# Kernel tuning notes

Measured on AMD Instinct MI355X. Metric: run time of the kernel, lower is better.

The kernel has to match this reference:

```python
import jax, jax.numpy as jnp
import numpy as np

N = 100000      # nodes
E = 1600000     # edges (avg degree 16)
F_IN = 128
H1, H2, C = 200, 50, 10


def _lin(key, fin, fout):
    # Glorot-uniform-ish init
    lim = (6.0 / (fin + fout)) ** 0.5
    return jax.random.uniform(key, (fin, fout), jnp.float32, -lim, lim)


def setup_inputs() -> dict:
    key = jax.random.key(0)
    ks = jax.random.split(key, 11)
    x = jax.random.normal(ks[0], (N, F_IN), jnp.float32)
    edge_index = jax.random.randint(ks[1], (2, E), 0, N, jnp.int32)
    return {
        "x": x,
        "edge_index": edge_index,
        "W_l1": _lin(ks[2], F_IN, H1), "b1": jnp.zeros((H1,), jnp.float32), "W_r1": _lin(ks[3], F_IN, H1),
        "W_l2": _lin(ks[4], H1, H2),   "b2": jnp.zeros((H2,), jnp.float32), "W_r2": _lin(ks[5], H1, H2),
        "W_l3": _lin(ks[6], H2, C),    "b3": jnp.zeros((C,), jnp.float32),  "W_r3": _lin(ks[7], H2, C),
    }


def _sage_conv_max(x, src, dst, W_l, b, W_r):
    # gather neighbor (source) features, scatter-max into destination nodes
    agg = jax.ops.segment_max(x[src], dst, num_segments=N)   # [N, F]
    agg = jnp.where(jnp.isfinite(agg), agg, 0.0)             # empty segments -> 0 (PyG behavior)
    return agg @ W_l + b + x @ W_r


def reference(x, edge_index, W_l1, b1, W_r1, W_l2, b2, W_r2, W_l3, b3, W_r3):
    src, dst = edge_index[0], edge_index[1]
    h = _sage_conv_max(x, src, dst, W_l1, b1, W_r1)   # [N, 200]
    h = _sage_conv_max(h, src, dst, W_l2, b2, W_r2)   # [N, 50]
    h = _sage_conv_max(h, src, dst, W_l3, b3, W_r3)   # [N, 10]
    return jax.nn.log_softmax(h, axis=1)
```

## Files before the change

### kernel.cpp

```cpp
#include <hip/hip_runtime.h>
#include <cstdint>
#include <cstddef>

#define N_NODES 100000
#define N_EDGES 1600000
#define F_IN    128
#define H1D     200
#define H2D     50
#define NCLS    10

#define P1 256
#define P2 416
#define P3 128
#define H2OFF 56

#define BSH 9
#define BMASK 511
#define NB 196
#define EPB 8192

typedef __attribute__((ext_vector_type(8))) short short8;
typedef __attribute__((ext_vector_type(4))) float f32x4;

__device__ __forceinline__ unsigned short f2b(float f) {
    union { float f; uint32_t u; } v; v.f = f;
    uint32_t u = v.u;
    return (unsigned short)((u + 0x7fffu + ((u >> 16) & 1u)) >> 16);
}
__device__ __forceinline__ float b2f(unsigned short b) {
    union { uint32_t u; float f; } v; v.u = ((uint32_t)b) << 16;
    return v.f;
}
__device__ __forceinline__ void upk(uint32_t p, float& a, float& b) {
    union { uint32_t u; float f; } lo, hi;
    lo.u = (p & 0xffffu) << 16;
    hi.u = p & 0xffff0000u;
    a = lo.f; b = hi.f;
}

__global__ void hist_kernel(const int* __restrict__ dst, int* __restrict__ deg, int E) {
    int e = blockIdx.x * blockDim.x + threadIdx.x;
    if (e < E) atomicAdd(&deg[dst[e]], 1);
}

__device__ __forceinline__ int block_excl_scan_256(int v, int* wsum) {
    const int tid = threadIdx.x;
    const int lane = tid & 63;
    const int wid = tid >> 6;
    int incl = v;
    #pragma unroll
    for (int off = 1; off < 64; off <<= 1) {
        int t = __shfl_up(incl, off, 64);
        if (lane >= off) incl += t;
    }
    if (lane == 63) wsum[wid] = incl;
    __syncthreads();
    if (tid == 0) {
        int s = 0;
        #pragma unroll
        for (int k = 0; k < 4; k++) { int t = wsum[k]; wsum[k] = s; s += t; }
    }
    __syncthreads();
    return wsum[wid] + incl - v;
}

__global__ __launch_bounds__(256) void scan_k1(const int* __restrict__ deg,
                                               int* __restrict__ row_ptr,
                                               int* __restrict__ bsum, int N) {
    __shared__ int wsum[4];
    const int tid = threadIdx.x;
    const int base = blockIdx.x * 1024 + tid * 4;
    int v[4];
    #pragma unroll
    for (int k = 0; k < 4; k++) v[k] = (base + k < N) ? deg[base + k] : 0;
    int t = v[0] + v[1] + v[2] + v[3];
    int texcl = block_excl_scan_256(t, wsum);
    int run = texcl;
    #pragma unroll
    for (int k = 0; k < 4; k++) {
        if (base + k < N) row_ptr[base + k] = run;
        run += v[k];
    }
    if (tid == 255) bsum[blockIdx.x] = texcl + t;
}

__global__ __launch_bounds__(256) void scan_k2(int* __restrict__ bsum, int NBLK) {
    __shared__ int wsum[4];
    const int tid = threadIdx.x;
    int v = (tid < NBLK) ? bsum[tid] : 0;
    int excl = block_excl_scan_256(v, wsum);
    if (tid < NBLK) bsum[tid] = excl;
}

__global__ __launch_bounds__(256) void scan_k3(int* __restrict__ row_ptr,
                                               const int* __restrict__ bsum, int N) {
    int add = bsum[blockIdx.x];
    int base = blockIdx.x * 1024 + threadIdx.x * 4;
    #pragma unroll
    for (int k = 0; k < 4; k++)
        if (base + k < N) row_ptr[base + k] += add;
}

__global__ void scan_k4(int* __restrict__ row_ptr, int* __restrict__ g_bcur, int N, int E) {
    int tid = threadIdx.x;
    if (tid == 0) row_ptr[N] = E;
    if (tid < NB) g_bcur[tid] = row_ptr[tid << BSH];
}

__global__ __launch_bounds__(256) void fill_pass1(const int* __restrict__ src,
                                                  const int* __restrict__ dst,
                                                  int* __restrict__ g_bcur,
                                                  uint32_t* __restrict__ staging, int E) {
    __shared__ int cnt[256];
    __shared__ int base_s[256];
    const int tid = threadIdx.x;
    const int base = blockIdx.x * EPB;
    cnt[tid] = 0;
    __syncthreads();
    #pragma unroll 4
    for (int i = 0; i < EPB / 256; i++) {
        int e = base + i * 256 + tid;
        if (e < E) atomicAdd(&cnt[dst[e] >> BSH], 1);
    }
    __syncthreads();
    int v = cnt[tid];
    if (v > 0) base_s[tid] = atomicAdd(&g_bcur[tid], v);
    cnt[tid] = 0;
    __syncthreads();
    #pragma unroll 4
    for (int i = 0; i < EPB / 256; i++) {
        int e = base + i * 256 + tid;
        if (e < E) {
            int d = dst[e], s = src[e];
            int b = d >> BSH;
            int r = atomicAdd(&cnt[b], 1);
            staging[base_s[b] + r] = ((uint32_t)s << BSH) | (uint32_t)(d & BMASK);
        }
    }
}

__global__ __launch_bounds__(256) void fill_pass2(const uint32_t* __restrict__ staging,
                                                  const int* __restrict__ row_ptr,
                                                  int* __restrict__ col_src, int N) {
    __shared__ int lcur[512];
    const int tid = threadIdx.x;
    const int nodeBase = blockIdx.x << BSH;
    for (int i = tid; i < 512; i += 256) {
        int node = nodeBase + i;
        lcur[i] = (node < N) ? row_ptr[node] : 0;
    }
    __syncthreads();
    const int lo = row_ptr[nodeBase];
    const int nodeEnd = min(nodeBase + 512, N);
    const int hi = row_ptr[nodeEnd];
    for (int j = lo + tid; j < hi; j += 256) {
        uint32_t rec = staging[j];
        int dl = rec & BMASK;
        int s  = (int)(rec >> BSH);
        int p = atomicAdd(&lcur[dl], 1);
        col_src[p] = s;
    }
}

__global__ void build_bt_kernel(const float* __restrict__ Wl, const float* __restrict__ Wr,
                                unsigned short* __restrict__ Bt,
                                int K1, int k2off, int K2, int M, int P) {
    int idx = blockIdx.x * blockDim.x + threadIdx.x;
    if (idx >= M * P) return;
    int m = idx / P, k = idx - m * P;
    float v = 0.0f;
    if (k < K1)                          v = Wl[(size_t)k * M + m];
    else if (k >= k2off && k < k2off+K2) v = Wr[(size_t)(k - k2off) * M + m];
    Bt[(size_t)m * P + k] = f2b(v);
}

__global__ void conv_x_kernel(const float* __restrict__ x, unsigned short* __restrict__ A1, int N) {
    int idx = blockIdx.x * blockDim.x + threadIdx.x;
    if (idx >= N * 32) return;
    int row = idx >> 5, c4 = (idx & 31) * 4;
    float4 v = *(const float4*)(x + (size_t)row * F_IN + c4);
    ushort4 o;
    o.x = f2b(v.x); o.y = f2b(v.y); o.z = f2b(v.z); o.w = f2b(v.w);
    *(ushort4*)(A1 + (size_t)row * P1 + F_IN + c4) = o;
}

__global__ void pad_zero_kernel(unsigned short* __restrict__ A, int pitch,
                                int begin, int width, int N) {
    int idx = blockIdx.x * blockDim.x + threadIdx.x;
    if (idx >= N * width) return;
    int r = idx / width, c = idx - r * width;
    A[(size_t)r * pitch + begin + c] = 0;
}

template <int F, int G>
__global__ __launch_bounds__(256) void agg_max_v2(
    const unsigned short* __restrict__ X, int xpitch,
    const int* __restrict__ row_ptr, const int* __restrict__ col_src,
    unsigned short* __restrict__ O, int opitch, int N) {
    static_assert(G == 8 || G == 16 || G == 32, "G must be 8/16/32");
    static_assert(G * 8 >= F, "group must cover F");
    const int wave = (blockIdx.x * blockDim.x + threadIdx.x) >> 6;
    const int lane = threadIdx.x & 63;
    if (wave >= N) return;
    const int beg = row_ptr[wave];
    const int end = row_ptr[wave + 1];
    constexpr int LOG2G = (G == 8) ? 3 : ((G == 16) ? 4 : 5);
    constexpr int EPW = 64 / G;
    const int l = lane & (G - 1);
    const int grp = lane >> LOG2G;
    const int f0 = l * 8;
    const bool act = (f0 < F);

    float m[8];
    #pragma unroll
    for (int i = 0; i < 8; i++) m[i] = -INFINITY;

    auto body = [&](int s) {
        if (act) {
            const uint4 v = *(const uint4*)(X + (size_t)s * xpitch + f0);
            float a, b;
            upk(v.x, a, b); m[0] = fmaxf(m[0], a); m[1] = fmaxf(m[1], b);
            upk(v.y, a, b); m[2] = fmaxf(m[2], a); m[3] = fmaxf(m[3], b);
            upk(v.z, a, b); m[4] = fmaxf(m[4], a); m[5] = fmaxf(m[5], b);
            upk(v.w, a, b); m[6] = fmaxf(m[6], a); m[7] = fmaxf(m[7], b);
        }
    };

    int j = beg + grp;
    for (; j + EPW < end; j += 2 * EPW) {
        int s0 = col_src[j];
        int s1 = col_src[j + EPW];
        body(s0);
        body(s1);
    }
    if (j < end) body(col_src[j]);

    #pragma unroll
    for (int off = G; off < 64; off <<= 1) {
        #pragma unroll
        for (int i = 0; i < 8; i++)
            m[i] = fmaxf(m[i], __shfl_xor(m[i], off, 64));
    }

    if (grp == 0 && act) {
        unsigned short* op = O + (size_t)wave * opitch;
        const bool empty = (beg == end);
        if (f0 + 8 <= F) {
            uint4 o = {0u, 0u, 0u, 0u};
            if (!empty) {
                o.x = (uint32_t)f2b(m[0]) | ((uint32_t)f2b(m[1]) << 16);
                o.y = (uint32_t)f2b(m[2]) | ((uint32_t)f2b(m[3]) << 16);
                o.z = (uint32_t)f2b(m[4]) | ((uint32_t)f2b(m[5]) << 16);
                o.w = (uint32_t)f2b(m[6]) | ((uint32_t)f2b(m[7]) << 16);
            }
            *(uint4*)(op + f0) = o;
        } else {
            for (int i = 0; f0 + i < F; i++)
                op[f0 + i] = empty ? (unsigned short)0 : f2b(m[i]);
        }
    }
}

__global__ __launch_bounds__(256) void gemm_mfma_kernel(
    const unsigned short* __restrict__ A, int P,
    const unsigned short* __restrict__ Bt,
    const float* __restrict__ bias,
    float* __restrict__ Cf,
    unsigned short* __restrict__ Cb, int cbPitch, int cbOff,
    int Nrows, int M) {
    __shared__ short As[64 * 40];
    __shared__ short Bs[64 * 40];
    const int tid = threadIdx.x;
    const int wv = tid >> 6;
    const int lane = tid & 63;
    const int q = lane >> 4;
    const int mi = lane & 15;
    const int rowBase = blockIdx.x * 64;
    const int colBase = blockIdx.y * 64;

    f32x4 acc[4];
    #pragma unroll
    for (int c = 0; c < 4; c++) acc[c] = (f32x4){0.f, 0.f, 0.f, 0.f};

    const int srow = tid >> 2;
    const int sseg = tid & 3;
    const int grow = rowBase + srow;
    const int gcol = colBase + srow;

    for (int kt = 0; kt < P; kt += 32) {
        uint4 va = {0u, 0u, 0u, 0u};
        uint4 vb = {0u, 0u, 0u, 0u};
        if (grow < Nrows) va = *(const uint4*)(A + (size_t)grow * P + kt + sseg * 8);
        if (gcol < M)     vb = *(const uint4*)(Bt + (size_t)gcol * P + kt + sseg * 8);
        *(uint4*)(&As[srow * 40 + sseg * 8]) = va;
        *(uint4*)(&Bs[srow * 40 + sseg * 8]) = vb;
        __syncthreads();
        short8 a = *(const short8*)(&As[(wv * 16 + mi) * 40 + q * 8]);
        #pragma unroll
        for (int c = 0; c < 4; c++) {
            short8 b = *(const short8*)(&Bs[(c * 16 + mi) * 40 + q * 8]);
            acc[c] = __builtin_amdgcn_mfma_f32_16x16x32_bf16(a, b, acc[c], 0, 0, 0);
        }
        __syncthreads();
    }

    #pragma unroll
    for (int c = 0; c < 4; c++) {
        int col = colBase + c * 16 + mi;
        if (col >= M) continue;
        float bv = bias[col];
        #pragma unroll
        for (int r = 0; r < 4; r++) {
            int row = rowBase + wv * 16 + q * 4 + r;
            if (row >= Nrows) continue;
            float v = acc[c][r] + bv;
            if (Cf) Cf[(size_t)row * M + col] = v;
            else    Cb[(size_t)row * cbPitch + cbOff + col] = f2b(v);
        }
    }
}

__global__ void logsoftmax_kernel(float* __restrict__ io, int N) {
    int n = blockIdx.x * blockDim.x + threadIdx.x;
    if (n >= N) return;
    float v[NCLS];
    float m = -INFINITY;
    #pragma unroll
    for (int i = 0; i < NCLS; i++) { v[i] = io[(size_t)n * NCLS + i]; m = fmaxf(m, v[i]); }
    float s = 0.0f;
    #pragma unroll
    for (int i = 0; i < NCLS; i++) s += expf(v[i] - m);
    float ls = logf(s);
    #pragma unroll
    for (int i = 0; i < NCLS; i++) io[(size_t)n * NCLS + i] = v[i] - m - ls;
}

extern "C" void kernel_launch(void* const* d_in, const int* in_sizes, int n_in,
                              void* d_out, int out_size, void* d_ws, size_t ws_size,
                              hipStream_t stream) {
    const float* x    = (const float*)d_in[0];
    const int*   eidx = (const int*)d_in[1];
    const float* Wl1  = (const float*)d_in[2];
    const float* b1   = (const float*)d_in[3];
    const float* Wr1  = (const float*)d_in[4];
    const float* Wl2  = (const float*)d_in[5];
    const float* b2   = (const float*)d_in[6];
    const float* Wr2  = (const float*)d_in[7];
    const float* Wl3  = (const float*)d_in[8];
    const float* b3   = (const float*)d_in[9];
    const float* Wr3  = (const float*)d_in[10];
    const int* srcp = eidx;
    const int* dstp = eidx + N_EDGES;
    float* out = (float*)d_out;
    (void)ws_size; (void)in_sizes; (void)n_in; (void)out_size;

    char* w = (char*)d_ws;
    size_t off = 0;
    auto alloc = [&](size_t bytes) -> char* {
        char* p = w + off;
        off += (bytes + 255) & ~(size_t)255;
        return p;
    };
    int* deg      = (int*)alloc(sizeof(int) * N_NODES);
    int* row_ptr  = (int*)alloc(sizeof(int) * (N_NODES + 1));
    int* col_src  = (int*)alloc(sizeof(int) * N_EDGES);
    uint32_t* staging = (uint32_t*)alloc(sizeof(uint32_t) * N_EDGES);
    int* bsum     = (int*)alloc(sizeof(int) * 128);
    int* g_bcur   = (int*)alloc(sizeof(int) * 256);
    unsigned short* A1  = (unsigned short*)alloc(sizeof(short) * (size_t)N_NODES * P1);
    unsigned short* A2  = (unsigned short*)alloc(sizeof(short) * (size_t)N_NODES * P2);
    unsigned short* A3  = (unsigned short*)alloc(sizeof(short) * (size_t)N_NODES * P3);
    unsigned short* Bt1 = (unsigned short*)alloc(sizeof(short) * H1D * P1);
    unsigned short* Bt2 = (unsigned short*)alloc(sizeof(short) * H2D * P2);
    unsigned short* Bt3 = (unsigned short*)alloc(sizeof(short) * NCLS * P3);

    const int SCAN_BLKS = (N_NODES + 1023) / 1024;
    hipMemsetAsync(deg, 0, sizeof(int) * N_NODES, stream);
    hist_kernel<<<(N_EDGES + 255) / 256, 256, 0, stream>>>(dstp, deg, N_EDGES);
    scan_k1<<<SCAN_BLKS, 256, 0, stream>>>(deg, row_ptr, bsum, N_NODES);
    scan_k2<<<1, 256, 0, stream>>>(bsum, SCAN_BLKS);
    scan_k3<<<SCAN_BLKS, 256, 0, stream>>>(row_ptr, bsum, N_NODES);
    scan_k4<<<1, 256, 0, stream>>>(row_ptr, g_bcur, N_NODES, N_EDGES);
    fill_pass1<<<(N_EDGES + EPB - 1) / EPB, 256, 0, stream>>>(srcp, dstp, g_bcur, staging, N_EDGES);
    fill_pass2<<<NB, 256, 0, stream>>>(staging, row_ptr, col_src, N_NODES);

    build_bt_kernel<<<(H1D * P1 + 255) / 256, 256, 0, stream>>>(Wl1, Wr1, Bt1, F_IN, F_IN, F_IN, H1D, P1);
    build_bt_kernel<<<(H2D * P2 + 255) / 256, 256, 0, stream>>>(Wl2, Wr2, Bt2, H1D, H1D, H1D, H2D, P2);
    build_bt_kernel<<<(NCLS * P3 + 255) / 256, 256, 0, stream>>>(Wl3, Wr3, Bt3, H2D, H2OFF, H2D, NCLS, P3);
    conv_x_kernel<<<(N_NODES * 32 + 255) / 256, 256, 0, stream>>>(x, A1, N_NODES);
    pad_zero_kernel<<<(N_NODES * 16 + 255) / 256, 256, 0, stream>>>(A2, P2, 2 * H1D, P2 - 2 * H1D, N_NODES);
    pad_zero_kernel<<<(N_NODES * 6 + 255) / 256, 256, 0, stream>>>(A3, P3, H2D, H2OFF - H2D, N_NODES);
    pad_zero_kernel<<<(N_NODES * 22 + 255) / 256, 256, 0, stream>>>(A3, P3, H2OFF + H2D, P3 - H2OFF - H2D, N_NODES);

    const int aggBlocks = (N_NODES + 3) / 4;
    const int rowTiles = (N_NODES + 63) / 64;

    agg_max_v2<F_IN, 16><<<aggBlocks, 256, 0, stream>>>(A1 + F_IN, P1, row_ptr, col_src, A1, P1, N_NODES);
    dim3 g1(rowTiles, (H1D + 63) / 64);
    gemm_mfma_kernel<<<g1, 256, 0, stream>>>(A1, P1, Bt1, b1, nullptr, A2, P2, H1D, N_NODES, H1D);

    agg_max_v2<H1D, 32><<<aggBlocks, 256, 0, stream>>>(A2 + H1D, P2, row_ptr, col_src, A2, P2, N_NODES);
    dim3 g2(rowTiles, 1);
    gemm_mfma_kernel<<<g2, 256, 0, stream>>>(A2, P2, Bt2, b2, nullptr, A3, P3, H2OFF, N_NODES, H2D);

    agg_max_v2<H2D, 8><<<aggBlocks, 256, 0, stream>>>(A3 + H2OFF, P3, row_ptr, col_src, A3, P3, N_NODES);
    dim3 g3(rowTiles, 1);
    gemm_mfma_kernel<<<g3, 256, 0, stream>>>(A3, P3, Bt3, b3, out, nullptr, 0, 0, N_NODES, NCLS);

    logsoftmax_kernel<<<(N_NODES + 255) / 256, 256, 0, stream>>>(out, N_NODES);
}
```

Baseline: 576.6 us.

## Restructure CSR build, unroll aggregation loads, widen GEMM tiles to full output

```diff
diff --git a/kernel.cpp b/kernel.cpp
--- a/kernel.cpp
+++ b/kernel.cpp
@@ -38,11 +38,6 @@
     a = lo.f; b = hi.f;
 }
 
-__global__ void hist_kernel(const int* __restrict__ dst, int* __restrict__ deg, int E) {
-    int e = blockIdx.x * blockDim.x + threadIdx.x;
-    if (e < E) atomicAdd(&deg[dst[e]], 1);
-}
-
 __device__ __forceinline__ int block_excl_scan_256(int v, int* wsum) {
     const int tid = threadIdx.x;
     const int lane = tid & 63;
@@ -64,53 +59,38 @@
     return wsum[wid] + incl - v;
 }
 
-__global__ __launch_bounds__(256) void scan_k1(const int* __restrict__ deg,
-                                               int* __restrict__ row_ptr,
-                                               int* __restrict__ bsum, int N) {
+__global__ __launch_bounds__(256) void csr_p0(const int* __restrict__ dst,
+                                              int* __restrict__ bcnt, int E) {
+    __shared__ int c[256];
+    const int tid = threadIdx.x;
+    c[tid] = 0;
+    __syncthreads();
+    const int base = blockIdx.x * EPB;
+    #pragma unroll 4
+    for (int i = 0; i < EPB / 256; i++) {
+        int e = base + i * 256 + tid;
+        if (e < E) atomicAdd(&c[dst[e] >> BSH], 1);
+    }
+    __syncthreads();
+    int v = c[tid];
+    if (v > 0) atomicAdd(&bcnt[tid], v);
+}
+
+__global__ __launch_bounds__(256) void csr_bscan(const int* __restrict__ bcnt,
+                                                 int* __restrict__ g_bbase,
+                                                 int* __restrict__ g_bcur) {
     __shared__ int wsum[4];
     const int tid = threadIdx.x;
-    const int base = blockIdx.x * 1024 + tid * 4;
-    int v[4];
-    #pragma unroll
-    for (int k = 0; k < 4; k++) v[k] = (base + k < N) ? deg[base + k] : 0;
-    int t = v[0] + v[1] + v[2] + v[3];
-    int texcl = block_excl_scan_256(t, wsum);
-    int run = texcl;
-    #pragma unroll
-    for (int k = 0; k < 4; k++) {
-        if (base + k < N) row_ptr[base + k] = run;
-        run += v[k];
-    }
-    if (tid == 255) bsum[blockIdx.x] = texcl + t;
-}
-
-__global__ __launch_bounds__(256) void scan_k2(int* __restrict__ bsum, int NBLK) {
-    __shared__ int wsum[4];
-    const int tid = threadIdx.x;
-    int v = (tid < NBLK) ? bsum[tid] : 0;
+    int v = (tid < NB) ? bcnt[tid] : 0;
     int excl = block_excl_scan_256(v, wsum);
-    if (tid < NBLK) bsum[tid] = excl;
-}
-
-__global__ __launch_bounds__(256) void scan_k3(int* __restrict__ row_ptr,
-                                               const int* __restrict__ bsum, int N) {
-    int add = bsum[blockIdx.x];
-    int base = blockIdx.x * 1024 + threadIdx.x * 4;
-    #pragma unroll
-    for (int k = 0; k < 4; k++)
-        if (base + k < N) row_ptr[base + k] += add;
-}
-
-__global__ void scan_k4(int* __restrict__ row_ptr, int* __restrict__ g_bcur, int N, int E) {
-    int tid = threadIdx.x;
-    if (tid == 0) row_ptr[N] = E;
-    if (tid < NB) g_bcur[tid] = row_ptr[tid << BSH];
-}
-
-__global__ __launch_bounds__(256) void fill_pass1(const int* __restrict__ src,
-                                                  const int* __restrict__ dst,
-                                                  int* __restrict__ g_bcur,
-                                                  uint32_t* __restrict__ staging, int E) {
+    if (tid < NB) { g_bbase[tid] = excl; g_bcur[tid] = excl; }
+    if (tid == NB) g_bbase[NB] = excl;
+}
+
+__global__ __launch_bounds__(256) void csr_p1(const int* __restrict__ src,
+                                              const int* __restrict__ dst,
+                                              int* __restrict__ g_bcur,
+                                              uint32_t* __restrict__ staging, int E) {
     __shared__ int cnt[256];
     __shared__ int base_s[256];
     const int tid = threadIdx.x;
@@ -139,27 +119,36 @@
     }
 }
 
-__global__ __launch_bounds__(256) void fill_pass2(const uint32_t* __restrict__ staging,
-                                                  const int* __restrict__ row_ptr,
-                                                  int* __restrict__ col_src, int N) {
-    __shared__ int lcur[512];
+__global__ __launch_bounds__(256) void csr_p2(const uint32_t* __restrict__ staging,
+                                              const int* __restrict__ g_bbase,
+                                              int* __restrict__ row_ptr,
+                                              int* __restrict__ col_src, int N, int E) {
+    __shared__ int cnt[512];
+    __shared__ int wsum[4];
     const int tid = threadIdx.x;
     const int nodeBase = blockIdx.x << BSH;
-    for (int i = tid; i < 512; i += 256) {
-        int node = nodeBase + i;
-        lcur[i] = (node < N) ? row_ptr[node] : 0;
-    }
-    __syncthreads();
-    const int lo = row_ptr[nodeBase];
-    const int nodeEnd = min(nodeBase + 512, N);
-    const int hi = row_ptr[nodeEnd];
+    cnt[tid] = 0; cnt[tid + 256] = 0;
+    __syncthreads();
+    const int lo = g_bbase[blockIdx.x];
+    const int hi = g_bbase[blockIdx.x + 1];
+    for (int j = lo + tid; j < hi; j += 256)
+        atomicAdd(&cnt[staging[j] & BMASK], 1);
+    __syncthreads();
+    int v0 = cnt[2 * tid], v1 = cnt[2 * tid + 1];
+    int pexcl = block_excl_scan_256(v0 + v1, wsum);
+    __syncthreads();
+    cnt[2 * tid]     = lo + pexcl;
+    cnt[2 * tid + 1] = lo + pexcl + v0;
+    int node0 = nodeBase + 2 * tid;
+    if (node0 < N)     row_ptr[node0]     = lo + pexcl;
+    if (node0 + 1 < N) row_ptr[node0 + 1] = lo + pexcl + v0;
+    __syncthreads();
     for (int j = lo + tid; j < hi; j += 256) {
         uint32_t rec = staging[j];
-        int dl = rec & BMASK;
-        int s  = (int)(rec >> BSH);
-        int p = atomicAdd(&lcur[dl], 1);
-        col_src[p] = s;
-    }
+        int p = atomicAdd(&cnt[rec & BMASK], 1);
+        col_src[p] = (int)(rec >> BSH);
+    }
+    if (blockIdx.x == 0 && tid == 0) row_ptr[N] = E;
 }
 
 __global__ void build_bt_kernel(const float* __restrict__ Wl, const float* __restrict__ Wr,
@@ -193,7 +182,7 @@
 }
 
 template <int F, int G>
-__global__ __launch_bounds__(256) void agg_max_v2(
+__global__ __launch_bounds__(256) void agg_max_v3(
     const unsigned short* __restrict__ X, int xpitch,
     const int* __restrict__ row_ptr, const int* __restrict__ col_src,
     unsigned short* __restrict__ O, int opitch, int N) {
@@ -215,9 +204,12 @@
     #pragma unroll
     for (int i = 0; i < 8; i++) m[i] = -INFINITY;
 
-    auto body = [&](int s) {
+    auto ld = [&](int s) -> uint4 {
+        if (act) return *(const uint4*)(X + (size_t)s * xpitch + f0);
+        return (uint4){0u, 0u, 0u, 0u};
+    };
+    auto mrg = [&](const uint4& v) {
         if (act) {
-            const uint4 v = *(const uint4*)(X + (size_t)s * xpitch + f0);
             float a, b;
             upk(v.x, a, b); m[0] = fmaxf(m[0], a); m[1] = fmaxf(m[1], b);
             upk(v.y, a, b); m[2] = fmaxf(m[2], a); m[3] = fmaxf(m[3], b);
@@ -227,13 +219,15 @@
     };
 
     int j = beg + grp;
-    for (; j + EPW < end; j += 2 * EPW) {
+    for (; j + 3 * EPW < end; j += 4 * EPW) {
         int s0 = col_src[j];
         int s1 = col_src[j + EPW];
-        body(s0);
-        body(s1);
-    }
-    if (j < end) body(col_src[j]);
+        int s2 = col_src[j + 2 * EPW];
+        int s3 = col_src[j + 3 * EPW];
+        uint4 v0 = ld(s0), v1 = ld(s1), v2 = ld(s2), v3 = ld(s3);
+        mrg(v0); mrg(v1); mrg(v2); mrg(v3);
+    }
+    for (; j < end; j += EPW) mrg(ld(col_src[j]));
 
     #pragma unroll
     for (int off = G; off < 64; off <<= 1) {
@@ -261,7 +255,8 @@
     }
 }
 
-__global__ __launch_bounds__(256) void gemm_mfma_kernel(
+template <int NCT>
+__global__ __launch_bounds__(256) void gemm_mfma_v2(
     const unsigned short* __restrict__ A, int P,
     const unsigned short* __restrict__ Bt,
     const float* __restrict__ bias,
@@ -269,35 +264,43 @@
     unsigned short* __restrict__ Cb, int cbPitch, int cbOff,
     int Nrows, int M) {
     __shared__ short As[64 * 40];
-    __shared__ short Bs[64 * 40];
+    __shared__ short Bs[NCT * 16 * 40];
     const int tid = threadIdx.x;
     const int wv = tid >> 6;
     const int lane = tid & 63;
     const int q = lane >> 4;
     const int mi = lane & 15;
     const int rowBase = blockIdx.x * 64;
-    const int colBase = blockIdx.y * 64;
-
-    f32x4 acc[4];
-    #pragma unroll
-    for (int c = 0; c < 4; c++) acc[c] = (f32x4){0.f, 0.f, 0.f, 0.f};
+
+    f32x4 acc[NCT];
+    #pragma unroll
+    for (int c = 0; c < NCT; c++) acc[c] = (f32x4){0.f, 0.f, 0.f, 0.f};
 
     const int srow = tid >> 2;
     const int sseg = tid & 3;
     const int grow = rowBase + srow;
-    const int gcol = colBase + srow;
+    constexpr int BSLOTS = NCT * 64;
+    constexpr int BITERS = (BSLOTS + 255) / 256;
 
     for (int kt = 0; kt < P; kt += 32) {
         uint4 va = {0u, 0u, 0u, 0u};
-        uint4 vb = {0u, 0u, 0u, 0u};
         if (grow < Nrows) va = *(const uint4*)(A + (size_t)grow * P + kt + sseg * 8);
-        if (gcol < M)     vb = *(const uint4*)(Bt + (size_t)gcol * P + kt + sseg * 8);
         *(uint4*)(&As[srow * 40 + sseg * 8]) = va;
-        *(uint4*)(&Bs[srow * 40 + sseg * 8]) = vb;
+        #pragma unroll
+        for (int i = 0; i < BITERS; i++) {
+            int slot = i * 256 + tid;
+            if (slot < BSLOTS) {
+                int br = slot >> 2;
+                int bs = slot & 3;
+                uint4 vb = {0u, 0u, 0u, 0u};
+                if (br < M) vb = *(const uint4*)(Bt + (size_t)br * P + kt + bs * 8);
+                *(uint4*)(&Bs[br * 40 + bs * 8]) = vb;
+            }
+        }
         __syncthreads();
         short8 a = *(const short8*)(&As[(wv * 16 + mi) * 40 + q * 8]);
         #pragma unroll
-        for (int c = 0; c < 4; c++) {
+        for (int c = 0; c < NCT; c++) {
             short8 b = *(const short8*)(&Bs[(c * 16 + mi) * 40 + q * 8]);
             acc[c] = __builtin_amdgcn_mfma_f32_16x16x32_bf16(a, b, acc[c], 0, 0, 0);
         }
@@ -305,8 +308,8 @@
     }
 
     #pragma unroll
-    for (int c = 0; c < 4; c++) {
-        int col = colBase + c * 16 + mi;
+    for (int c = 0; c < NCT; c++) {
+        int col = c * 16 + mi;
         if (col >= M) continue;
         float bv = bias[col];
         #pragma unroll
@@ -361,12 +364,12 @@
         off += (bytes + 255) & ~(size_t)255;
         return p;
     };
-    int* deg      = (int*)alloc(sizeof(int) * N_NODES);
+    int* bcnt     = (int*)alloc(sizeof(int) * 256);
+    int* g_bbase  = (int*)alloc(sizeof(int) * 256);
+    int* g_bcur   = (int*)alloc(sizeof(int) * 256);
     int* row_ptr  = (int*)alloc(sizeof(int) * (N_NODES + 1));
     int* col_src  = (int*)alloc(sizeof(int) * N_EDGES);
     uint32_t* staging = (uint32_t*)alloc(sizeof(uint32_t) * N_EDGES);
-    int* bsum     = (int*)alloc(sizeof(int) * 128);
-    int* g_bcur   = (int*)alloc(sizeof(int) * 256);
     unsigned short* A1  = (unsigned short*)alloc(sizeof(short) * (size_t)N_NODES * P1);
     unsigned short* A2  = (unsigned short*)alloc(sizeof(short) * (size_t)N_NODES * P2);
     unsigned short* A3  = (unsigned short*)alloc(sizeof(short) * (size_t)N_NODES * P3);
@@ -374,15 +377,12 @@
     unsigned short* Bt2 = (unsigned short*)alloc(sizeof(short) * H2D * P2);
     unsigned short* Bt3 = (unsigned short*)alloc(sizeof(short) * NCLS * P3);
 
-    const int SCAN_BLKS = (N_NODES + 1023) / 1024;
-    hipMemsetAsync(deg, 0, sizeof(int) * N_NODES, stream);
-    hist_kernel<<<(N_EDGES + 255) / 256, 256, 0, stream>>>(dstp, deg, N_EDGES);
-    scan_k1<<<SCAN_BLKS, 256, 0, stream>>>(deg, row_ptr, bsum, N_NODES);
-    scan_k2<<<1, 256, 0, stream>>>(bsum, SCAN_BLKS);
-    scan_k3<<<SCAN_BLKS, 256, 0, stream>>>(row_ptr, bsum, N_NODES);
-    scan_k4<<<1, 256, 0, stream>>>(row_ptr, g_bcur, N_NODES, N_EDGES);
-    fill_pass1<<<(N_EDGES + EPB - 1) / EPB, 256, 0, stream>>>(srcp, dstp, g_bcur, staging, N_EDGES);
-    fill_pass2<<<NB, 256, 0, stream>>>(staging, row_ptr, col_src, N_NODES);
+    const int EDGE_BLKS = (N_EDGES + EPB - 1) / EPB;
+    hipMemsetAsync(bcnt, 0, sizeof(int) * 256, stream);
+    csr_p0<<<EDGE_BLKS, 256, 0, stream>>>(dstp, bcnt, N_EDGES);
+    csr_bscan<<<1, 256, 0, stream>>>(bcnt, g_bbase, g_bcur);
+    csr_p1<<<EDGE_BLKS, 256, 0, stream>>>(srcp, dstp, g_bcur, staging, N_EDGES);
+    csr_p2<<<NB, 256, 0, stream>>>(staging, g_bbase, row_ptr, col_src, N_NODES, N_EDGES);
 
     build_bt_kernel<<<(H1D * P1 + 255) / 256, 256, 0, stream>>>(Wl1, Wr1, Bt1, F_IN, F_IN, F_IN, H1D, P1);
     build_bt_kernel<<<(H2D * P2 + 255) / 256, 256, 0, stream>>>(Wl2, Wr2, Bt2, H1D, H1D, H1D, H2D, P2);
@@ -395,17 +395,14 @@
     const int aggBlocks = (N_NODES + 3) / 4;
     const int rowTiles = (N_NODES + 63) / 64;
 
-    agg_max_v2<F_IN, 16><<<aggBlocks, 256, 0, stream>>>(A1 + F_IN, P1, row_ptr, col_src, A1, P1, N_NODES);
-    dim3 g1(rowTiles, (H1D + 63) / 64);
-    gemm_mfma_kernel<<<g1, 256, 0, stream>>>(A1, P1, Bt1, b1, nullptr, A2, P2, H1D, N_NODES, H1D);
-
-    agg_max_v2<H1D, 32><<<aggBlocks, 256, 0, stream>>>(A2 + H1D, P2, row_ptr, col_src, A2, P2, N_NODES);
-    dim3 g2(rowTiles, 1);
-    gemm_mfma_kernel<<<g2, 256, 0, stream>>>(A2, P2, Bt2, b2, nullptr, A3, P3, H2OFF, N_NODES, H2D);
-
-    agg_max_v2<H2D, 8><<<aggBlocks, 256, 0, stream>>>(A3 + H2OFF, P3, row_ptr, col_src, A3, P3, N_NODES);
-    dim3 g3(rowTiles, 1);
-    gemm_mfma_kernel<<<g3, 256, 0, stream>>>(A3, P3, Bt3, b3, out, nullptr, 0, 0, N_NODES, NCLS);
+    agg_max_v3<F_IN, 16><<<aggBlocks, 256, 0, stream>>>(A1 + F_IN, P1, row_ptr, col_src, A1, P1, N_NODES);
+    gemm_mfma_v2<13><<<rowTiles, 256, 0, stream>>>(A1, P1, Bt1, b1, nullptr, A2, P2, H1D, N_NODES, H1D);
+
+    agg_max_v3<H1D, 32><<<aggBlocks, 256, 0, stream>>>(A2 + H1D, P2, row_ptr, col_src, A2, P2, N_NODES);
+    gemm_mfma_v2<4><<<rowTiles, 256, 0, stream>>>(A2, P2, Bt2, b2, nullptr, A3, P3, H2OFF, N_NODES, H2D);
+
+    agg_max_v3<H2D, 8><<<aggBlocks, 256, 0, stream>>>(A3 + H2OFF, P3, row_ptr, col_src, A3, P3, N_NODES);
+    gemm_mfma_v2<1><<<rowTiles, 256, 0, stream>>>(A3, P3, Bt3, b3, out, nullptr, 0, 0, N_NODES, NCLS);
 
     logsoftmax_kernel<<<(N_NODES + 255) / 256, 256, 0, stream>>>(out, N_NODES);
 }
```

Measured after the change: 524.8 us. -9.0%, faster.
